# Optimization experiments

Measured on AMD Instinct MI355X. Metric: run time of the kernel, lower is better.

## Reference

```python
import jax, jax.numpy as jnp
import numpy as np

N = 50000          # nodes
E = 1600000        # edges (avg degree 32)
D_IN = 128
D_OUT = 128
NUM_ETYPES = 8
K = 10             # propagation hops
ALPHA = 0.1
EDGE_HID = 32


def setup_inputs() -> dict:
    key = jax.random.key(0)
    ks = jax.random.split(key, 14)
    def lin(k, fan_in, fan_out):
        lim = 1.0 / np.sqrt(fan_in)
        return jax.random.uniform(k, (fan_in, fan_out), jnp.float32, -lim, lim)
    return {
        "feat": jax.random.normal(ks[0], (N, D_IN), jnp.float32),
        "e_feat": jax.random.randint(ks[1], (E,), 0, NUM_ETYPES),
        "src": jax.random.randint(ks[2], (E,), 0, N),
        "dst": jax.random.randint(ks[3], (E,), 0, N),
        "edge_embeds": jax.random.normal(ks[4], (NUM_ETYPES, D_IN), jnp.float32),
        "We1": lin(ks[5], D_IN, EDGE_HID),
        "be1": jnp.zeros((EDGE_HID,), jnp.float32),
        "We2": lin(ks[6], EDGE_HID, 1),
        "be2": jnp.zeros((1,), jnp.float32),
        "W1": lin(ks[7], D_IN, D_OUT),
        "b1": jnp.zeros((D_OUT,), jnp.float32),
        "W2": lin(ks[8], D_OUT, D_OUT),
        "b2": jnp.zeros((D_OUT,), jnp.float32),
    }


def reference(feat, e_feat, src, dst, edge_embeds, We1, be1, We2, be2, W1, b1, W2, b2):
    # degree-based symmetric normalization (clamped at 1)
    ones_e = jnp.ones((E,), feat.dtype)
    out_deg = jax.ops.segment_sum(ones_e, src, num_segments=N)
    in_deg = jax.ops.segment_sum(ones_e, dst, num_segments=N)
    src_norm = jnp.power(jnp.maximum(out_deg, 1.0), -0.5)[:, None]  # [N,1]
    dst_norm = jnp.power(jnp.maximum(in_deg, 1.0), -0.5)[:, None]   # [N,1]

    # per-edge gate: sigmoid(MLP(embedding(etype)))  -> [E,1]
    eh = jax.nn.gelu(edge_embeds[e_feat] @ We1 + be1, approximate=False)
    e_gate = jax.nn.sigmoid(eh @ We2 + be2)
    w = 1.0 + e_gate  # edge_drop p=0 -> identity on the ones tensor

    feat_0 = feat

    def hop(h, _):
        h = h * src_norm                                   # [N,D]
        m = h[src] * w                                     # [E,D] gather + gate
        agg = jax.ops.segment_sum(m, dst, num_segments=N)  # [N,D] scatter-sum
        h = agg * dst_norm
        h = (1.0 - ALPHA) * h + ALPHA * feat_0             # residual mix
        return h, None

    feat, _ = jax.lax.scan(hop, feat, None, length=K)

    # output MLP: Linear -> GELU -> Linear
    return jax.nn.gelu(feat @ W1 + b1, approximate=False) @ W2 + b2
```

## Files before the change

kernel.cpp:

```cpp
#include <hip/hip_runtime.h>
#include <cmath>


#define NNODES 50000
#define NEDGES 1600000
#define DD 128
#define KHOPS 10
#define ALPHA 0.1f

#define RS 16384
#define NRANGE 4
#define NSLICE 64
#define SLICE_E (NEDGES / NSLICE)

typedef short short8 __attribute__((ext_vector_type(8)));
typedef float f32x4 __attribute__((ext_vector_type(4)));

static __device__ __forceinline__ unsigned bf16rne(float x) {
    unsigned u = __float_as_uint(x);
    return (u + 0x7FFFu + ((u >> 16) & 1u)) >> 16;
}
static __device__ __forceinline__ float bf_lo(unsigned w) { return __uint_as_float(w << 16); }
static __device__ __forceinline__ float bf_hi(unsigned w) { return __uint_as_float(w & 0xFFFF0000u); }

__global__ __launch_bounds__(256) void gate_kernel(const float* __restrict__ emb,
                                                   const float* __restrict__ We1,
                                                   const float* __restrict__ be1,
                                                   const float* __restrict__ We2,
                                                   const float* __restrict__ be2,
                                                   float* __restrict__ gate) {
    int tid = threadIdx.x;
    int t = tid >> 5, j = tid & 31;
    float a = be1[j];
#pragma unroll 8
    for (int k = 0; k < DD; k++)
        a += emb[t * DD + k] * We1[k * 32 + j];
    float g = 0.5f * a * (1.0f + erff(a * 0.70710678118654752f));
    float p = g * We2[j];
#pragma unroll
    for (int m = 16; m >= 1; m >>= 1) p += __shfl_xor(p, m, 32);
    if (j == 0) gate[t] = 1.0f + 1.0f / (1.0f + expf(-(p + be2[0])));
}

__global__ __launch_bounds__(256) void wconv_kernel(const float* __restrict__ W1,
                                                    const float* __restrict__ W2,
                                                    unsigned short* __restrict__ w1b,
                                                    unsigned short* __restrict__ w2b) {
    int i = blockIdx.x * 256 + threadIdx.x;
    if (i < DD * DD) {
        w1b[i] = (unsigned short)bf16rne(W1[i]);
        w2b[i] = (unsigned short)bf16rne(W2[i]);
    }
}

__global__ __launch_bounds__(256) void hist_kernel(const int* __restrict__ key,
                                                   int* __restrict__ cnt) {
    __shared__ int h[RS];
    int b = blockIdx.x, r = blockIdx.y;
    int lo = r * RS;
    int hi = lo + RS; if (hi > NNODES) hi = NNODES;
    for (int i = threadIdx.x; i < RS; i += 256) h[i] = 0;
    __syncthreads();
    const int4* p = (const int4*)(key + b * SLICE_E);
    for (int i = threadIdx.x; i < SLICE_E / 4; i += 256) {
        int4 v = p[i];
        if (v.x >= lo && v.x < hi) atomicAdd(&h[v.x - lo], 1);
        if (v.y >= lo && v.y < hi) atomicAdd(&h[v.y - lo], 1);
        if (v.z >= lo && v.z < hi) atomicAdd(&h[v.z - lo], 1);
        if (v.w >= lo && v.w < hi) atomicAdd(&h[v.w - lo], 1);
    }
    __syncthreads();
    int n = hi - lo;
    for (int i = threadIdx.x; i < n; i += 256)
        cnt[(size_t)b * NNODES + lo + i] = h[i];
}

__global__ __launch_bounds__(256) void reduce_scan_kernel(const int* __restrict__ cnt_in,
                                                          const int* __restrict__ cnt_out,
                                                          int* __restrict__ incnt,
                                                          int* __restrict__ outcnt,
                                                          int* __restrict__ excl,
                                                          int* __restrict__ bsum, int N) {
    __shared__ int sh[256];
    int t = threadIdx.x;
    int g = blockIdx.x * 256 + t;
    int a = 0, b = 0;
    if (g < N) {
        for (int x = 0; x < NSLICE; x++) {
            a += cnt_in[(size_t)x * NNODES + g];
            b += cnt_out[(size_t)x * NNODES + g];
        }
        incnt[g] = a;
        outcnt[g] = b;
    }
    int v = a;
    sh[t] = v;
    __syncthreads();
    for (int off = 1; off < 256; off <<= 1) {
        int u = 0;
        if (t >= off) u = sh[t - off];
        __syncthreads();
        sh[t] += u;
        __syncthreads();
    }
    if (g < N) excl[g] = sh[t] - v;
    if (t == 255) bsum[blockIdx.x] = sh[255];
}

__global__ __launch_bounds__(256) void scan2_kernel(int* __restrict__ bsum, int nb) {
    __shared__ int sh[256];
    int t = threadIdx.x;
    int v = (t < nb) ? bsum[t] : 0;
    sh[t] = v;
    __syncthreads();
    for (int off = 1; off < 256; off <<= 1) {
        int u = 0;
        if (t >= off) u = sh[t - off];
        __syncthreads();
        sh[t] += u;
        __syncthreads();
    }
    if (t < nb) bsum[t] = sh[t] - v;
}
__global__ __launch_bounds__(256) void scan3_kernel(const int* __restrict__ excl,
                                                    const int* __restrict__ bsum,
                                                    int* __restrict__ row_ptr, int N, int E) {
    int g = blockIdx.x * 256 + threadIdx.x;
    if (g < N) row_ptr[g] = excl[g] + bsum[g >> 8];
    if (g == N) row_ptr[N] = E;
}

__global__ __launch_bounds__(256) void base_kernel(const int* __restrict__ row_ptr,
                                                   const int* __restrict__ cnt_in,
                                                   int* __restrict__ base_part, int N) {
    int n = blockIdx.x * 256 + threadIdx.x;
    if (n >= N) return;
    int run = row_ptr[n];
    for (int b = 0; b < NSLICE; b++) {
        base_part[(size_t)b * NNODES + n] = run;
        run += cnt_in[(size_t)b * NNODES + n];
    }
}

__global__ __launch_bounds__(256) void scatter2_kernel(const int* __restrict__ src,
                                                       const int* __restrict__ dst,
                                                       const int* __restrict__ ef,
                                                       const int* __restrict__ base_part,
                                                       int* __restrict__ epay) {
    __shared__ int cur[RS];
    int b = blockIdx.x, r = blockIdx.y;
    int lo = r * RS;
    int hi = lo + RS; if (hi > NNODES) hi = NNODES;
    int n = hi - lo;
    for (int i = threadIdx.x; i < n; i += 256)
        cur[i] = base_part[(size_t)b * NNODES + lo + i];
    __syncthreads();
    int off = b * SLICE_E;
    const int4* pd = (const int4*)(dst + off);
    const int4* ps = (const int4*)(src + off);
    const int4* pf = (const int4*)(ef + off);
    for (int i = threadIdx.x; i < SLICE_E / 4; i += 256) {
        int4 d = pd[i];
        int4 s = ps[i];
        int4 f = pf[i];
        int dv[4] = {d.x, d.y, d.z, d.w};
        int sv[4] = {s.x, s.y, s.z, s.w};
        int fv[4] = {f.x, f.y, f.z, f.w};
#pragma unroll
        for (int u = 0; u < 4; u++) {
            if (dv[u] >= lo && dv[u] < hi) {
                int pos = atomicAdd(&cur[dv[u] - lo], 1);
                epay[pos] = sv[u] | (fv[u] << 16);
            }
        }
    }
}

__global__ void scale_kernel(const float* __restrict__ feat, const int* __restrict__ outcnt,
                             unsigned* __restrict__ g0, int N) {
    int i = blockIdx.x * blockDim.x + threadIdx.x;
    if (i >= N * 32) return;
    int row = i >> 5;
    int oc = outcnt[row]; if (oc < 1) oc = 1;
    float sn = rsqrtf((float)oc);
    float4 v = ((const float4*)feat)[i];
    uint2 o;
    o.x = bf16rne(v.x * sn) | (bf16rne(v.y * sn) << 16);
    o.y = bf16rne(v.z * sn) | (bf16rne(v.w * sn) << 16);
    ((uint2*)g0)[i] = o;
}

__global__ __launch_bounds__(256) void hop_kernel(const unsigned* __restrict__ g_in,
                                                  const float* __restrict__ feat0,
                                                  const int* __restrict__ incnt,
                                                  const int* __restrict__ outcnt,
                                                  const float* __restrict__ gate_g,
                                                  const int* __restrict__ row_ptr,
                                                  const int* __restrict__ epay,
                                                  unsigned* __restrict__ g_out,
                                                  int N, int last) {
    __shared__ float gateL[8];
    if (threadIdx.x < 8) gateL[threadIdx.x] = gate_g[threadIdx.x];
    __syncthreads();
    int half = threadIdx.x >> 5;
    int lane = threadIdx.x & 31;
    int node = blockIdx.x * 8 + half;
    if (node >= N) return;
    int beg = row_ptr[node], end = row_ptr[node + 1];
    const uint2* gp = (const uint2*)g_in;
    float a0 = 0.f, a1 = 0.f, a2 = 0.f, a3 = 0.f;
    for (int base = beg; base < end; base += 32) {
        int n = end - base; if (n > 32) n = 32;
        int p = 0;
        if (lane < n) p = epay[base + lane];
        int j = 0;
        for (; j + 12 <= n; j += 12) {
            float cg[12];
            uint2 v[12];
#pragma unroll
            for (int u = 0; u < 12; u++) {
                int pj = __shfl(p, j + u, 32);
                cg[u] = gateL[(unsigned)pj >> 16];
                v[u] = gp[((unsigned)(pj & 0xFFFF) << 5) + lane];
            }
#pragma unroll
            for (int u = 0; u < 12; u++) {
                a0 += cg[u] * bf_lo(v[u].x); a1 += cg[u] * bf_hi(v[u].x);
                a2 += cg[u] * bf_lo(v[u].y); a3 += cg[u] * bf_hi(v[u].y);
            }
        }
        for (; j + 8 <= n; j += 8) {
            float cg[8];
            uint2 v[8];
#pragma unroll
            for (int u = 0; u < 8; u++) {
                int pj = __shfl(p, j + u, 32);
                cg[u] = gateL[(unsigned)pj >> 16];
                v[u] = gp[((unsigned)(pj & 0xFFFF) << 5) + lane];
            }
#pragma unroll
            for (int u = 0; u < 8; u++) {
                a0 += cg[u] * bf_lo(v[u].x); a1 += cg[u] * bf_hi(v[u].x);
                a2 += cg[u] * bf_lo(v[u].y); a3 += cg[u] * bf_hi(v[u].y);
            }
        }
        for (; j < n; j++) {
            int pj = __shfl(p, j, 32);
            float c = gateL[(unsigned)pj >> 16];
            uint2 v = gp[((unsigned)(pj & 0xFFFF) << 5) + lane];
            a0 += c * bf_lo(v.x); a1 += c * bf_hi(v.x);
            a2 += c * bf_lo(v.y); a3 += c * bf_hi(v.y);
        }
    }
    int ic = incnt[node]; if (ic < 1) ic = 1;
    float dn = rsqrtf((float)ic) * (1.0f - ALPHA);
    float4 fv = *(const float4*)(feat0 + (size_t)node * DD + lane * 4);
    float h0 = dn * a0 + ALPHA * fv.x;
    float h1 = dn * a1 + ALPHA * fv.y;
    float h2 = dn * a2 + ALPHA * fv.z;
    float h3 = dn * a3 + ALPHA * fv.w;
    float sc = 1.0f;
    if (!last) { int oc = outcnt[node]; if (oc < 1) oc = 1; sc = rsqrtf((float)oc); }
    uint2 o;
    o.x = bf16rne(h0 * sc) | (bf16rne(h1 * sc) << 16);
    o.y = bf16rne(h2 * sc) | (bf16rne(h3 * sc) << 16);
    ((uint2*)g_out)[(size_t)node * 32 + lane] = o;
}

#define ASTR 136
__global__ __launch_bounds__(256) void mlp_mfma_kernel(const unsigned short* __restrict__ in,
                                                       const unsigned short* __restrict__ Wb,
                                                       const float* __restrict__ bias,
                                                       void* __restrict__ outp,
                                                       int N, int mode) {
    __shared__ unsigned short As[64 * ASTR];
    __shared__ unsigned short Bs[128 * ASTR];
    int tid = threadIdx.x;
    int row0 = blockIdx.x * 64;
    for (int i = tid; i < 64 * 16; i += 256) {
        int r = i >> 4, c8 = i & 15;
        int gr = row0 + r; if (gr >= N) gr = N - 1;
        uint4 v = *(const uint4*)(in + (size_t)gr * DD + c8 * 8);
        *(uint4*)&As[r * ASTR + c8 * 8] = v;
    }
    for (int i = tid; i < 128 * 128; i += 256) {
        int k = i >> 7, n = i & 127;
        Bs[n * ASTR + k] = Wb[i];
    }
    __syncthreads();

    int wv = tid >> 6, lane = tid & 63;
    int m = lane & 15, quad = lane >> 4;
    const unsigned short* arow = &As[(16 * wv + m) * ASTR + quad * 8];
    f32x4 acc[8];
#pragma unroll
    for (int t = 0; t < 8; t++) {
        const unsigned short* brow = &Bs[(t * 16 + m) * ASTR + quad * 8];
        f32x4 c = {0.f, 0.f, 0.f, 0.f};
#pragma unroll
        for (int s = 0; s < 4; s++) {
            short8 a = *(const short8*)(arow + s * 32);
            short8 b = *(const short8*)(brow + s * 32);
            c = __builtin_amdgcn_mfma_f32_16x16x32_bf16(a, b, c, 0, 0, 0);
        }
        acc[t] = c;
    }
#pragma unroll
    for (int t = 0; t < 8; t++) {
        float bv = bias[t * 16 + m];
#pragma unroll
        for (int r = 0; r < 4; r++) {
            int grow = row0 + 16 * wv + quad * 4 + r;
            if (grow >= N) continue;
            float v = acc[t][r] + bv;
            size_t oidx = (size_t)grow * DD + t * 16 + m;
            if (mode == 0) {
                v = 0.5f * v * (1.0f + erff(v * 0.70710678118654752f));
                ((unsigned short*)outp)[oidx] = (unsigned short)bf16rne(v);
            } else {
                ((float*)outp)[oidx] = v;
            }
        }
    }
}

extern "C" void kernel_launch(void* const* d_in, const int* in_sizes, int n_in,
                              void* d_out, int out_size, void* d_ws, size_t ws_size,
                              hipStream_t stream) {
    const float* feat = (const float*)d_in[0];
    const int*   e_feat = (const int*)d_in[1];
    const int*   src = (const int*)d_in[2];
    const int*   dst = (const int*)d_in[3];
    const float* emb = (const float*)d_in[4];
    const float* We1 = (const float*)d_in[5];
    const float* be1 = (const float*)d_in[6];
    const float* We2 = (const float*)d_in[7];
    const float* be2 = (const float*)d_in[8];
    const float* W1  = (const float*)d_in[9];
    const float* b1  = (const float*)d_in[10];
    const float* W2  = (const float*)d_in[11];
    const float* b2  = (const float*)d_in[12];
    float* out = (float*)d_out;

    const int N = NNODES, E = NEDGES;
    const int NBLK = (N + 255) / 256;
    char* ws = (char*)d_ws;
    size_t off = 0;
    unsigned* ga = (unsigned*)(ws + off);  off += (size_t)N * 256;
    unsigned* gb = (unsigned*)(ws + off);  off += (size_t)N * 256;
    int*   epay = (int*)(ws + off);        off += (size_t)E * 4;
    int*   row_ptr = (int*)(ws + off);     off += (size_t)(N + 1) * 4;
    int*   excl = (int*)(ws + off);        off += (size_t)N * 4;
    int*   bsum = (int*)(ws + off);        off += 256 * 4;
    int*   cnts = (int*)(ws + off);        off += (size_t)2 * N * 4;
    int*   cnt_in = (int*)(ws + off);      off += (size_t)NSLICE * N * 4;
    int*   cnt_out = (int*)(ws + off);     off += (size_t)NSLICE * N * 4;
    int*   base_part = (int*)(ws + off);   off += (size_t)NSLICE * N * 4;
    unsigned short* w1b = (unsigned short*)(ws + off); off += (size_t)DD * DD * 2;
    unsigned short* w2b = (unsigned short*)(ws + off); off += (size_t)DD * DD * 2;
    float* gate = (float*)(ws + off);      off += 64;
    int* incnt  = cnts;
    int* outcnt = cnts + N;

    gate_kernel<<<1, 256, 0, stream>>>(emb, We1, be1, We2, be2, gate);
    wconv_kernel<<<(DD * DD + 255) / 256, 256, 0, stream>>>(W1, W2, w1b, w2b);
    dim3 hg(NSLICE, NRANGE);
    hist_kernel<<<hg, 256, 0, stream>>>(dst, cnt_in);
    hist_kernel<<<hg, 256, 0, stream>>>(src, cnt_out);
    reduce_scan_kernel<<<NBLK, 256, 0, stream>>>(cnt_in, cnt_out, incnt, outcnt,
                                                 excl, bsum, N);
    scan2_kernel<<<1, 256, 0, stream>>>(bsum, NBLK);
    scan3_kernel<<<(N + 256) / 256 + 1, 256, 0, stream>>>(excl, bsum, row_ptr, N, E);
    base_kernel<<<(N + 255) / 256, 256, 0, stream>>>(row_ptr, cnt_in, base_part, N);
    scatter2_kernel<<<hg, 256, 0, stream>>>(src, dst, e_feat, base_part, epay);
    scale_kernel<<<(N * 32 + 255) / 256, 256, 0, stream>>>(feat, outcnt, ga, N);

    const unsigned* gin = ga;
    unsigned* gout = gb;
    for (int k = 0; k < KHOPS; k++) {
        int last = (k == KHOPS - 1);
        hop_kernel<<<(N + 7) / 8, 256, 0, stream>>>(gin, feat, incnt, outcnt, gate,
                                                    row_ptr, epay, gout, N, last);
        gin = gout;
        gout = (gout == ga) ? gb : ga;
    }
    const unsigned short* hfin = (const unsigned short*)gin;
    unsigned short* hidden = (unsigned short*)gout;
    mlp_mfma_kernel<<<(N + 63) / 64, 256, 0, stream>>>(hfin, w1b, b1, hidden, N, 0);
    mlp_mfma_kernel<<<(N + 63) / 64, 256, 0, stream>>>(hidden, w2b, b2, out, N, 1);
}
```

Measured before the change: 776.9 us.

## Fuse degree histograms with packed 16-bit counters, merge scan kernels, bf16 residual

The two degree histogram passes become one kernel that reads dst and src together. Its shared-memory counters are packed as 16-bit halves so each block covers twice the node range with half as many range blocks. The scan3 step is folded into base_kernel. The residual term ALPHA*feat0 is precomputed once as bf16, so each hop reads half the bytes for it. The cost is extra rounding error in the residual and the risk that a 16-bit counter overflows if one slice holds more than 65535 edges for a node.

Result: faster. 758.5 us (-2.4%).

```diff
diff --git a/kernel.cpp b/kernel.cpp
--- a/kernel.cpp
+++ b/kernel.cpp
@@ -8,8 +8,8 @@
 #define KHOPS 10
 #define ALPHA 0.1f
 
-#define RS 16384
-#define NRANGE 4
+#define RS 32768
+#define NRANGE 2
 #define NSLICE 64
 #define SLICE_E (NEDGES / NSLICE)
 
@@ -53,26 +53,42 @@
     }
 }
 
-__global__ __launch_bounds__(256) void hist_kernel(const int* __restrict__ key,
-                                                   int* __restrict__ cnt) {
-    __shared__ int h[RS];
+__global__ __launch_bounds__(256) void hist_kernel(const int* __restrict__ dst,
+                                                   const int* __restrict__ src,
+                                                   int* __restrict__ cnt_in,
+                                                   int* __restrict__ cnt_out) {
+    __shared__ unsigned hin[RS / 2];
+    __shared__ unsigned hout[RS / 2];
     int b = blockIdx.x, r = blockIdx.y;
     int lo = r * RS;
     int hi = lo + RS; if (hi > NNODES) hi = NNODES;
-    for (int i = threadIdx.x; i < RS; i += 256) h[i] = 0;
-    __syncthreads();
-    const int4* p = (const int4*)(key + b * SLICE_E);
+    for (int i = threadIdx.x; i < RS / 2; i += 256) { hin[i] = 0; hout[i] = 0; }
+    __syncthreads();
+    const int4* pd = (const int4*)(dst + b * SLICE_E);
+    const int4* ps = (const int4*)(src + b * SLICE_E);
     for (int i = threadIdx.x; i < SLICE_E / 4; i += 256) {
-        int4 v = p[i];
-        if (v.x >= lo && v.x < hi) atomicAdd(&h[v.x - lo], 1);
-        if (v.y >= lo && v.y < hi) atomicAdd(&h[v.y - lo], 1);
-        if (v.z >= lo && v.z < hi) atomicAdd(&h[v.z - lo], 1);
-        if (v.w >= lo && v.w < hi) atomicAdd(&h[v.w - lo], 1);
+        int4 d = pd[i];
+        int4 s = ps[i];
+        int dv[4] = {d.x, d.y, d.z, d.w};
+        int sv[4] = {s.x, s.y, s.z, s.w};
+#pragma unroll
+        for (int u = 0; u < 4; u++) {
+            if (dv[u] >= lo && dv[u] < hi) {
+                int k = dv[u] - lo;
+                atomicAdd(&hin[k >> 1], 1u << ((k & 1) * 16));
+            }
+            if (sv[u] >= lo && sv[u] < hi) {
+                int k = sv[u] - lo;
+                atomicAdd(&hout[k >> 1], 1u << ((k & 1) * 16));
+            }
+        }
     }
     __syncthreads();
     int n = hi - lo;
-    for (int i = threadIdx.x; i < n; i += 256)
-        cnt[(size_t)b * NNODES + lo + i] = h[i];
+    for (int i = threadIdx.x; i < n; i += 256) {
+        cnt_in[(size_t)b * NNODES + lo + i]  = (hin[i >> 1]  >> ((i & 1) * 16)) & 0xFFFF;
+        cnt_out[(size_t)b * NNODES + lo + i] = (hout[i >> 1] >> ((i & 1) * 16)) & 0xFFFF;
+    }
 }
 
 __global__ __launch_bounds__(256) void reduce_scan_kernel(const int* __restrict__ cnt_in,
@@ -122,20 +138,17 @@
     }
     if (t < nb) bsum[t] = sh[t] - v;
 }
-__global__ __launch_bounds__(256) void scan3_kernel(const int* __restrict__ excl,
-                                                    const int* __restrict__ bsum,
-                                                    int* __restrict__ row_ptr, int N, int E) {
-    int g = blockIdx.x * 256 + threadIdx.x;
-    if (g < N) row_ptr[g] = excl[g] + bsum[g >> 8];
-    if (g == N) row_ptr[N] = E;
-}
-
-__global__ __launch_bounds__(256) void base_kernel(const int* __restrict__ row_ptr,
+
+__global__ __launch_bounds__(256) void base_kernel(const int* __restrict__ excl,
+                                                   const int* __restrict__ bsum,
                                                    const int* __restrict__ cnt_in,
-                                                   int* __restrict__ base_part, int N) {
+                                                   int* __restrict__ row_ptr,
+                                                   int* __restrict__ base_part, int N, int E) {
     int n = blockIdx.x * 256 + threadIdx.x;
+    if (n == N) row_ptr[N] = E;
     if (n >= N) return;
-    int run = row_ptr[n];
+    int run = excl[n] + bsum[n >> 8];
+    row_ptr[n] = run;
     for (int b = 0; b < NSLICE; b++) {
         base_part[(size_t)b * NNODES + n] = run;
         run += cnt_in[(size_t)b * NNODES + n];
@@ -177,21 +190,24 @@
 }
 
 __global__ void scale_kernel(const float* __restrict__ feat, const int* __restrict__ outcnt,
-                             unsigned* __restrict__ g0, int N) {
+                             unsigned* __restrict__ g0, unsigned* __restrict__ af0, int N) {
     int i = blockIdx.x * blockDim.x + threadIdx.x;
     if (i >= N * 32) return;
     int row = i >> 5;
     int oc = outcnt[row]; if (oc < 1) oc = 1;
     float sn = rsqrtf((float)oc);
     float4 v = ((const float4*)feat)[i];
-    uint2 o;
+    uint2 o, a;
     o.x = bf16rne(v.x * sn) | (bf16rne(v.y * sn) << 16);
     o.y = bf16rne(v.z * sn) | (bf16rne(v.w * sn) << 16);
+    a.x = bf16rne(v.x * ALPHA) | (bf16rne(v.y * ALPHA) << 16);
+    a.y = bf16rne(v.z * ALPHA) | (bf16rne(v.w * ALPHA) << 16);
     ((uint2*)g0)[i] = o;
+    ((uint2*)af0)[i] = a;
 }
 
 __global__ __launch_bounds__(256) void hop_kernel(const unsigned* __restrict__ g_in,
-                                                  const float* __restrict__ feat0,
+                                                  const unsigned* __restrict__ af0,
                                                   const int* __restrict__ incnt,
                                                   const int* __restrict__ outcnt,
                                                   const float* __restrict__ gate_g,
@@ -254,17 +270,17 @@
     }
     int ic = incnt[node]; if (ic < 1) ic = 1;
     float dn = rsqrtf((float)ic) * (1.0f - ALPHA);
-    float4 fv = *(const float4*)(feat0 + (size_t)node * DD + lane * 4);
-    float h0 = dn * a0 + ALPHA * fv.x;
-    float h1 = dn * a1 + ALPHA * fv.y;
-    float h2 = dn * a2 + ALPHA * fv.z;
-    float h3 = dn * a3 + ALPHA * fv.w;
+    uint2 af = ((const uint2*)af0)[((unsigned)node << 5) + lane];
+    float h0 = dn * a0 + bf_lo(af.x);
+    float h1 = dn * a1 + bf_hi(af.x);
+    float h2 = dn * a2 + bf_lo(af.y);
+    float h3 = dn * a3 + bf_hi(af.y);
     float sc = 1.0f;
     if (!last) { int oc = outcnt[node]; if (oc < 1) oc = 1; sc = rsqrtf((float)oc); }
     uint2 o;
     o.x = bf16rne(h0 * sc) | (bf16rne(h1 * sc) << 16);
     o.y = bf16rne(h2 * sc) | (bf16rne(h3 * sc) << 16);
-    ((uint2*)g_out)[(size_t)node * 32 + lane] = o;
+    ((uint2*)g_out)[((unsigned)node << 5) + lane] = o;
 }
 
 #define ASTR 136
@@ -348,6 +364,7 @@
     size_t off = 0;
     unsigned* ga = (unsigned*)(ws + off);  off += (size_t)N * 256;
     unsigned* gb = (unsigned*)(ws + off);  off += (size_t)N * 256;
+    unsigned* af0 = (unsigned*)(ws + off); off += (size_t)N * 256;
     int*   epay = (int*)(ws + off);        off += (size_t)E * 4;
     int*   row_ptr = (int*)(ws + off);     off += (size_t)(N + 1) * 4;
     int*   excl = (int*)(ws + off);        off += (size_t)N * 4;
@@ -365,21 +382,20 @@
     gate_kernel<<<1, 256, 0, stream>>>(emb, We1, be1, We2, be2, gate);
     wconv_kernel<<<(DD * DD + 255) / 256, 256, 0, stream>>>(W1, W2, w1b, w2b);
     dim3 hg(NSLICE, NRANGE);
-    hist_kernel<<<hg, 256, 0, stream>>>(dst, cnt_in);
-    hist_kernel<<<hg, 256, 0, stream>>>(src, cnt_out);
+    hist_kernel<<<hg, 256, 0, stream>>>(dst, src, cnt_in, cnt_out);
     reduce_scan_kernel<<<NBLK, 256, 0, stream>>>(cnt_in, cnt_out, incnt, outcnt,
                                                  excl, bsum, N);
     scan2_kernel<<<1, 256, 0, stream>>>(bsum, NBLK);
-    scan3_kernel<<<(N + 256) / 256 + 1, 256, 0, stream>>>(excl, bsum, row_ptr, N, E);
-    base_kernel<<<(N + 255) / 256, 256, 0, stream>>>(row_ptr, cnt_in, base_part, N);
+    base_kernel<<<(N + 256) / 256 + 1, 256, 0, stream>>>(excl, bsum, cnt_in,
+                                                         row_ptr, base_part, N, E);
     scatter2_kernel<<<hg, 256, 0, stream>>>(src, dst, e_feat, base_part, epay);
-    scale_kernel<<<(N * 32 + 255) / 256, 256, 0, stream>>>(feat, outcnt, ga, N);
+    scale_kernel<<<(N * 32 + 255) / 256, 256, 0, stream>>>(feat, outcnt, ga, af0, N);
 
     const unsigned* gin = ga;
     unsigned* gout = gb;
     for (int k = 0; k < KHOPS; k++) {
         int last = (k == KHOPS - 1);
-        hop_kernel<<<(N + 7) / 8, 256, 0, stream>>>(gin, feat, incnt, outcnt, gate,
+        hop_kernel<<<(N + 7) / 8, 256, 0, stream>>>(gin, af0, incnt, outcnt, gate,
                                                     row_ptr, epay, gout, N, last);
         gin = gout;
         gout = (gout == ga) ? gb : ga;
```
